# Kernel optimization log

Measured on AMD Instinct MI355X. Metric: run time of the kernel, lower is better.

Reference implementation:

```python
import jax, jax.numpy as jnp
import numpy as np

# Neighbor offsets (di, dj) implied by each 3x3 kernel: out_j = gray - shift(gray, di, dj)
# kernel0..kernel7 as defined in the torch module (center weight +1, one neighbor -1)
OFFSETS = [(0, -1), (1, -1), (1, 0), (1, 1), (0, 1), (-1, 1), (-1, 0), (-1, -1)]
EPS = 1e-5  # torch InstanceNorm2d default


def setup_inputs() -> dict:
    key = jax.random.key(0)
    x = jax.random.uniform(key, (8, 3, 1024, 1024), dtype=jnp.float32)
    return {"x": x}


def _ltpe(x):
    # RGB -> gray, [B,1,H,W]
    g = (0.3 * x[:, 0] + 0.59 * x[:, 1] + 0.11 * x[:, 2])[:, None]
    B, _, H, W = g.shape
    gp = jnp.pad(g, ((0, 0), (0, 0), (1, 1), (1, 1)))  # zero pad = conv padding=1
    out = jnp.zeros_like(g)
    for j, (di, dj) in enumerate(OFFSETS):
        nb = gp[:, :, 1 + di:1 + di + H, 1 + dj:1 + dj + W]
        d = (g - nb + 1.0) * 0.5          # (conv_out + 1) * 0.5
        out = out + d * (float(2 ** j) / 255.0)
    # InstanceNorm2d(1): per (b, c) mean/biased-var over spatial dims, no affine
    mean = jnp.mean(out, axis=(2, 3), keepdims=True)
    var = jnp.var(out, axis=(2, 3), keepdims=True)
    out = (out - mean) * jax.lax.rsqrt(var + EPS)
    return jnp.concatenate([out, out, out], axis=1)  # [B,3,H,W]


def reference(x):
    return _ltpe(x)
```

## Files before the change

### kernel.cpp

```cpp
#include <hip/hip_runtime.h>
#include <math.h>

constexpr int H = 1024, W = 1024, B = 8;
constexpr int NPIX = H * W;

__device__ __forceinline__ float grayat(const float* __restrict__ xb, int r, int c) {
    const float* p = xb + (size_t)r * W + c;
    return 0.3f * p[0] + 0.59f * p[NPIX] + 0.11f * p[2 * NPIX];
}

__global__ __launch_bounds__(256)
void ltpe_stage1(const float* __restrict__ x, float* __restrict__ out,
                 float2* __restrict__ part)
{
    const int b    = blockIdx.y;
    const int k    = blockIdx.x;
    const int r    = ((k & 7) << 7) | (k >> 3);
    const int tid  = threadIdx.x;
    const int c    = tid << 2;
    const int lane = tid & 63;

    const float* xb = x + (size_t)b * 3 * NPIX;

    float4 g[3];
    #pragma unroll
    for (int dr = 0; dr < 3; ++dr) {
        const int rr = r + dr - 1;
        float4 q0 = {0.f,0.f,0.f,0.f}, q1 = q0, q2 = q0;
        if ((unsigned)rr < (unsigned)H) {
            const float* p = xb + (size_t)rr * W + c;
            q0 = *reinterpret_cast<const float4*>(p);
            q1 = *reinterpret_cast<const float4*>(p + NPIX);
            q2 = *reinterpret_cast<const float4*>(p + 2 * NPIX);
        }
        g[dr].x = 0.3f * q0.x + 0.59f * q1.x + 0.11f * q2.x;
        g[dr].y = 0.3f * q0.y + 0.59f * q1.y + 0.11f * q2.y;
        g[dr].z = 0.3f * q0.z + 0.59f * q1.z + 0.11f * q2.z;
        g[dr].w = 0.3f * q0.w + 0.59f * q1.w + 0.11f * q2.w;
    }

    float gl[3], gr[3];
    #pragma unroll
    for (int dr = 0; dr < 3; ++dr) {
        gl[dr] = __shfl_up(g[dr].w, 1);
        gr[dr] = __shfl_down(g[dr].x, 1);
    }
    if (lane == 0) {
        #pragma unroll
        for (int dr = 0; dr < 3; ++dr) {
            const int rr = r + dr - 1;
            gl[dr] = (c > 0 && (unsigned)rr < (unsigned)H) ? grayat(xb, rr, c - 1) : 0.f;
        }
    }
    if (lane == 63) {
        #pragma unroll
        for (int dr = 0; dr < 3; ++dr) {
            const int rr = r + dr - 1;
            gr[dr] = (c + 4 < W && (unsigned)rr < (unsigned)H) ? grayat(xb, rr, c + 4) : 0.f;
        }
    }

    float up[6], mi[6], dn[6];
    up[0]=gl[0]; up[1]=g[0].x; up[2]=g[0].y; up[3]=g[0].z; up[4]=g[0].w; up[5]=gr[0];
    mi[0]=gl[1]; mi[1]=g[1].x; mi[2]=g[1].y; mi[3]=g[1].z; mi[4]=g[1].w; mi[5]=gr[1];
    dn[0]=gl[2]; dn[1]=g[2].x; dn[2]=g[2].y; dn[3]=g[2].z; dn[4]=g[2].w; dn[5]=gr[2];

    constexpr float w0 = 1.f/255.f,  w1 = 2.f/255.f,  w2 = 4.f/255.f,  w3 = 8.f/255.f,
                    w4 = 16.f/255.f, w5 = 32.f/255.f, w6 = 64.f/255.f, w7 = 128.f/255.f;
    float tv[4];
    #pragma unroll
    for (int kk = 0; kk < 4; ++kk) {
        float s = w0 * mi[kk];
        s = fmaf(w1, dn[kk],     s);
        s = fmaf(w2, dn[kk + 1], s);
        s = fmaf(w3, dn[kk + 2], s);
        s = fmaf(w4, mi[kk + 2], s);
        s = fmaf(w5, up[kk + 2], s);
        s = fmaf(w6, up[kk + 1], s);
        s = fmaf(w7, up[kk],     s);
        tv[kk] = 0.5f * mi[kk + 1] + 0.5f - 0.5f * s;
    }

    float4 t4 = {tv[0], tv[1], tv[2], tv[3]};
    *reinterpret_cast<float4*>(out + (size_t)b * 3 * NPIX + (size_t)r * W + c) = t4;

    float s  = tv[0] + tv[1] + tv[2] + tv[3];
    float ss = tv[0]*tv[0] + tv[1]*tv[1] + tv[2]*tv[2] + tv[3]*tv[3];
    #pragma unroll
    for (int off = 32; off >= 1; off >>= 1) {
        s  += __shfl_down(s, off);
        ss += __shfl_down(ss, off);
    }
    __shared__ float2 wred[4];
    if (lane == 0) wred[tid >> 6] = make_float2(s, ss);
    __syncthreads();
    if (tid == 0) {
        float2 a0 = wred[0], a1 = wred[1], a2 = wred[2], a3 = wred[3];
        part[(size_t)b * H + k] = make_float2(a0.x + a1.x + a2.x + a3.x,
                                              a0.y + a1.y + a2.y + a3.y);
    }
}

__global__ __launch_bounds__(256)
void ltpe_stageB(float* __restrict__ out, const float2* __restrict__ part)
{
    const int b   = blockIdx.y;
    const int r   = blockIdx.x;
    const int tid = threadIdx.x;
    const int lane = tid & 63;

    const float4* pp = reinterpret_cast<const float4*>(part + (size_t)b * H);
    const float4 u = pp[tid * 2];
    const float4 v = pp[tid * 2 + 1];
    double s  = (double)u.x + (double)u.z + (double)v.x + (double)v.z;
    double ss = (double)u.y + (double)u.w + (double)v.y + (double)v.w;
    #pragma unroll
    for (int off = 32; off >= 1; off >>= 1) {
        s  += __shfl_down(s, off);
        ss += __shfl_down(ss, off);
    }
    __shared__ double red[8];
    __shared__ float2 mv;
    const int wv = tid >> 6;
    if (lane == 0) { red[wv] = s; red[4 + wv] = ss; }
    __syncthreads();
    if (tid == 0) {
        const double S  = red[0] + red[1] + red[2] + red[3];
        const double SS = red[4] + red[5] + red[6] + red[7];
        const double n    = (double)NPIX;
        const double mean = S / n;
        const double var  = SS / n - mean * mean;
        mv = make_float2((float)mean, (float)(1.0 / sqrt(var + 1e-5)));
    }
    __syncthreads();
    const float mean = mv.x, rstd = mv.y;

    const size_t base = (size_t)b * 3 * NPIX + (size_t)r * W + (tid << 2);
    const float4 t4 = *reinterpret_cast<const float4*>(out + base);
    float4 y;
    y.x = (t4.x - mean) * rstd;
    y.y = (t4.y - mean) * rstd;
    y.z = (t4.z - mean) * rstd;
    y.w = (t4.w - mean) * rstd;
    *reinterpret_cast<float4*>(out + base)            = y;
    *reinterpret_cast<float4*>(out + base + NPIX)     = y;
    *reinterpret_cast<float4*>(out + base + 2 * NPIX) = y;
}

extern "C" void kernel_launch(void* const* d_in, const int* in_sizes, int n_in,
                              void* d_out, int out_size, void* d_ws, size_t ws_size,
                              hipStream_t stream)
{
    const float* x = (const float*)d_in[0];
    float* out = (float*)d_out;
    float2* part = (float2*)d_ws;

    ltpe_stage1<<<dim3(H, B), 256, 0, stream>>>(x, out, part);
    ltpe_stageB<<<dim3(H, B), 256, 0, stream>>>(out, part);
}
```

Measured before the change: 54.36 us.

## Process two rows per block with async global-to-LDS loads for halo reuse

Stage 1 now computes two output rows per block. It loads the four needed input rows for all three channels straight into LDS with global_load_lds, so the shared row is read once instead of recomputed by separate blocks, and the per-lane edge reloads are replaced by LDS neighbour reads. Input read traffic drops from 3 rows per output row to 2. Partial sums halve, and stage B reduces 512 partials per image. The cost is 48KB of LDS per block, which lowers occupancy, plus a block-wide sync before any compute can start.

Result: faster. 51.65 us (-5.0%).

```diff
diff --git a/kernel.cpp b/kernel.cpp
--- a/kernel.cpp
+++ b/kernel.cpp
@@ -3,117 +3,125 @@
 
 constexpr int H = 1024, W = 1024, B = 8;
 constexpr int NPIX = H * W;
+constexpr int ROWS = 2;
+constexpr int RG   = H / ROWS;
 
-__device__ __forceinline__ float grayat(const float* __restrict__ xb, int r, int c) {
-    const float* p = xb + (size_t)r * W + c;
-    return 0.3f * p[0] + 0.59f * p[NPIX] + 0.11f * p[2 * NPIX];
+__device__ __forceinline__ void gload_lds16(const float* g, float* l) {
+    __builtin_amdgcn_global_load_lds(
+        (const __attribute__((address_space(1))) void*)g,
+        (__attribute__((address_space(3))) void*)l, 16, 0, 0);
 }
 
 __global__ __launch_bounds__(256)
 void ltpe_stage1(const float* __restrict__ x, float* __restrict__ out,
                  float2* __restrict__ part)
 {
-    const int b    = blockIdx.y;
-    const int k    = blockIdx.x;
-    const int r    = ((k & 7) << 7) | (k >> 3);
-    const int tid  = threadIdx.x;
-    const int c    = tid << 2;
-    const int lane = tid & 63;
-
+    __shared__ float lds[4][3][W];
+    const int b   = blockIdx.y;
+    const int k   = blockIdx.x;
+    const int kg  = ((k & 7) << 6) | (k >> 3);
+    const int r0  = kg * ROWS;
+    const int tid = threadIdx.x;
+    const int w   = tid >> 6;
+    const int l   = tid & 63;
+    const int c   = tid << 2;
     const float* xb = x + (size_t)b * 3 * NPIX;
 
-    float4 g[3];
     #pragma unroll
-    for (int dr = 0; dr < 3; ++dr) {
-        const int rr = r + dr - 1;
-        float4 q0 = {0.f,0.f,0.f,0.f}, q1 = q0, q2 = q0;
+    for (int s = 0; s < 4; ++s) {
+        const int rr = r0 - 1 + s;
         if ((unsigned)rr < (unsigned)H) {
-            const float* p = xb + (size_t)rr * W + c;
-            q0 = *reinterpret_cast<const float4*>(p);
-            q1 = *reinterpret_cast<const float4*>(p + NPIX);
-            q2 = *reinterpret_cast<const float4*>(p + 2 * NPIX);
-        }
-        g[dr].x = 0.3f * q0.x + 0.59f * q1.x + 0.11f * q2.x;
-        g[dr].y = 0.3f * q0.y + 0.59f * q1.y + 0.11f * q2.y;
-        g[dr].z = 0.3f * q0.z + 0.59f * q1.z + 0.11f * q2.z;
-        g[dr].w = 0.3f * q0.w + 0.59f * q1.w + 0.11f * q2.w;
-    }
-
-    float gl[3], gr[3];
-    #pragma unroll
-    for (int dr = 0; dr < 3; ++dr) {
-        gl[dr] = __shfl_up(g[dr].w, 1);
-        gr[dr] = __shfl_down(g[dr].x, 1);
-    }
-    if (lane == 0) {
-        #pragma unroll
-        for (int dr = 0; dr < 3; ++dr) {
-            const int rr = r + dr - 1;
-            gl[dr] = (c > 0 && (unsigned)rr < (unsigned)H) ? grayat(xb, rr, c - 1) : 0.f;
+            #pragma unroll
+            for (int ch = 0; ch < 3; ++ch) {
+                const float* gp = xb + (size_t)ch * NPIX + (size_t)rr * W + (w << 8) + (l << 2);
+                gload_lds16(gp, &lds[s][ch][w << 8]);
+            }
+        } else {
+            const float4 z = make_float4(0.f, 0.f, 0.f, 0.f);
+            #pragma unroll
+            for (int ch = 0; ch < 3; ++ch)
+                *reinterpret_cast<float4*>(&lds[s][ch][c]) = z;
         }
     }
-    if (lane == 63) {
-        #pragma unroll
-        for (int dr = 0; dr < 3; ++dr) {
-            const int rr = r + dr - 1;
-            gr[dr] = (c + 4 < W && (unsigned)rr < (unsigned)H) ? grayat(xb, rr, c + 4) : 0.f;
-        }
+    __syncthreads();
+
+    const int ql = (tid == 0)   ? 0   : tid - 1;
+    const int qr = (tid == 255) ? 255 : tid + 1;
+    float g6[4][6];
+    #pragma unroll
+    for (int s = 0; s < 4; ++s) {
+        const float4 o0 = *reinterpret_cast<const float4*>(&lds[s][0][c]);
+        const float4 o1 = *reinterpret_cast<const float4*>(&lds[s][1][c]);
+        const float4 o2 = *reinterpret_cast<const float4*>(&lds[s][2][c]);
+        const float4 l0 = *reinterpret_cast<const float4*>(&lds[s][0][ql << 2]);
+        const float4 l1 = *reinterpret_cast<const float4*>(&lds[s][1][ql << 2]);
+        const float4 l2 = *reinterpret_cast<const float4*>(&lds[s][2][ql << 2]);
+        const float4 rq0 = *reinterpret_cast<const float4*>(&lds[s][0][qr << 2]);
+        const float4 rq1 = *reinterpret_cast<const float4*>(&lds[s][1][qr << 2]);
+        const float4 rq2 = *reinterpret_cast<const float4*>(&lds[s][2][qr << 2]);
+        g6[s][1] = 0.3f * o0.x + 0.59f * o1.x + 0.11f * o2.x;
+        g6[s][2] = 0.3f * o0.y + 0.59f * o1.y + 0.11f * o2.y;
+        g6[s][3] = 0.3f * o0.z + 0.59f * o1.z + 0.11f * o2.z;
+        g6[s][4] = 0.3f * o0.w + 0.59f * o1.w + 0.11f * o2.w;
+        g6[s][0] = (tid == 0)   ? 0.f : 0.3f * l0.w  + 0.59f * l1.w  + 0.11f * l2.w;
+        g6[s][5] = (tid == 255) ? 0.f : 0.3f * rq0.x + 0.59f * rq1.x + 0.11f * rq2.x;
     }
-
-    float up[6], mi[6], dn[6];
-    up[0]=gl[0]; up[1]=g[0].x; up[2]=g[0].y; up[3]=g[0].z; up[4]=g[0].w; up[5]=gr[0];
-    mi[0]=gl[1]; mi[1]=g[1].x; mi[2]=g[1].y; mi[3]=g[1].z; mi[4]=g[1].w; mi[5]=gr[1];
-    dn[0]=gl[2]; dn[1]=g[2].x; dn[2]=g[2].y; dn[3]=g[2].z; dn[4]=g[2].w; dn[5]=gr[2];
 
     constexpr float w0 = 1.f/255.f,  w1 = 2.f/255.f,  w2 = 4.f/255.f,  w3 = 8.f/255.f,
                     w4 = 16.f/255.f, w5 = 32.f/255.f, w6 = 64.f/255.f, w7 = 128.f/255.f;
-    float tv[4];
+    float s = 0.f, ss = 0.f;
+    float* ob = out + (size_t)b * 3 * NPIX + (size_t)r0 * W + c;
     #pragma unroll
-    for (int kk = 0; kk < 4; ++kk) {
-        float s = w0 * mi[kk];
-        s = fmaf(w1, dn[kk],     s);
-        s = fmaf(w2, dn[kk + 1], s);
-        s = fmaf(w3, dn[kk + 2], s);
-        s = fmaf(w4, mi[kk + 2], s);
-        s = fmaf(w5, up[kk + 2], s);
-        s = fmaf(w6, up[kk + 1], s);
-        s = fmaf(w7, up[kk],     s);
-        tv[kk] = 0.5f * mi[kk + 1] + 0.5f - 0.5f * s;
+    for (int rr = 0; rr < ROWS; ++rr) {
+        const float (&up)[6] = g6[rr];
+        const float (&mi)[6] = g6[rr + 1];
+        const float (&dn)[6] = g6[rr + 2];
+        float tv[4];
+        #pragma unroll
+        for (int kk = 0; kk < 4; ++kk) {
+            float sv = w0 * mi[kk];
+            sv = fmaf(w1, dn[kk],     sv);
+            sv = fmaf(w2, dn[kk + 1], sv);
+            sv = fmaf(w3, dn[kk + 2], sv);
+            sv = fmaf(w4, mi[kk + 2], sv);
+            sv = fmaf(w5, up[kk + 2], sv);
+            sv = fmaf(w6, up[kk + 1], sv);
+            sv = fmaf(w7, up[kk],     sv);
+            tv[kk] = 0.5f * mi[kk + 1] + 0.5f - 0.5f * sv;
+            s += tv[kk];
+            ss = fmaf(tv[kk], tv[kk], ss);
+        }
+        float4 t4 = {tv[0], tv[1], tv[2], tv[3]};
+        *reinterpret_cast<float4*>(ob + (size_t)rr * W) = t4;
     }
 
-    float4 t4 = {tv[0], tv[1], tv[2], tv[3]};
-    *reinterpret_cast<float4*>(out + (size_t)b * 3 * NPIX + (size_t)r * W + c) = t4;
-
-    float s  = tv[0] + tv[1] + tv[2] + tv[3];
-    float ss = tv[0]*tv[0] + tv[1]*tv[1] + tv[2]*tv[2] + tv[3]*tv[3];
     #pragma unroll
     for (int off = 32; off >= 1; off >>= 1) {
         s  += __shfl_down(s, off);
         ss += __shfl_down(ss, off);
     }
     __shared__ float2 wred[4];
-    if (lane == 0) wred[tid >> 6] = make_float2(s, ss);
+    if (l == 0) wred[w] = make_float2(s, ss);
     __syncthreads();
     if (tid == 0) {
         float2 a0 = wred[0], a1 = wred[1], a2 = wred[2], a3 = wred[3];
-        part[(size_t)b * H + k] = make_float2(a0.x + a1.x + a2.x + a3.x,
-                                              a0.y + a1.y + a2.y + a3.y);
+        part[(size_t)b * RG + kg] = make_float2(a0.x + a1.x + a2.x + a3.x,
+                                                a0.y + a1.y + a2.y + a3.y);
     }
 }
 
 __global__ __launch_bounds__(256)
 void ltpe_stageB(float* __restrict__ out, const float2* __restrict__ part)
 {
-    const int b   = blockIdx.y;
-    const int r   = blockIdx.x;
-    const int tid = threadIdx.x;
+    const int b    = blockIdx.y;
+    const int r    = blockIdx.x;
+    const int tid  = threadIdx.x;
     const int lane = tid & 63;
 
-    const float4* pp = reinterpret_cast<const float4*>(part + (size_t)b * H);
-    const float4 u = pp[tid * 2];
-    const float4 v = pp[tid * 2 + 1];
-    double s  = (double)u.x + (double)u.z + (double)v.x + (double)v.z;
-    double ss = (double)u.y + (double)u.w + (double)v.y + (double)v.w;
+    const float4* pp = reinterpret_cast<const float4*>(part + (size_t)b * RG);
+    const float4 u = pp[tid];
+    double s  = (double)u.x + (double)u.z;
+    double ss = (double)u.y + (double)u.w;
     #pragma unroll
     for (int off = 32; off >= 1; off >>= 1) {
         s  += __shfl_down(s, off);
@@ -155,6 +163,6 @@
     float* out = (float*)d_out;
     float2* part = (float2*)d_ws;
 
-    ltpe_stage1<<<dim3(H, B), 256, 0, stream>>>(x, out, part);
+    ltpe_stage1<<<dim3(RG, B), 256, 0, stream>>>(x, out, part);
     ltpe_stageB<<<dim3(H, B), 256, 0, stream>>>(out, part);
 }
```
